# Optimization experiments

Hardware: AMD Instinct MI355X
Metric: run time of the kernel (lower is better)

The kernel has to match this reference:

```python
import jax, jax.numpy as jnp
import numpy as np
from jax import lax

B, N, G, K, D = 32, 32768, 64, 32, 384
EPS = 1e-5


def _fps(xyz, npoint):
    # Farthest point sampling; deterministic start at index 0 (original uses randint).
    b, n, _ = xyz.shape
    def step(carry, _):
        distance, farthest = carry
        centroid = jnp.take_along_axis(xyz, farthest[:, None, None], axis=1)  # (B,1,3)
        dist = jnp.sum((xyz - centroid) ** 2, axis=-1)                        # (B,N)
        distance = jnp.minimum(distance, dist)
        new_far = jnp.argmax(distance, axis=-1)
        return (distance, new_far), farthest
    init = (jnp.full((b, n), 1e10, xyz.dtype), jnp.zeros((b,), jnp.int32))
    _, cents = lax.scan(step, init, None, length=npoint)  # (npoint, B)
    return cents.T  # (B, npoint)


def _bn(h, g, bta, m, v):
    # inference-mode BatchNorm over channel (last) dim
    return (h - m) * (g * lax.rsqrt(v + EPS)) + bta


def setup_inputs() -> dict:
    key = jax.random.key(0)
    ks = jax.random.split(key, 5)
    xyz = jax.random.normal(ks[0], (B, N, 3), jnp.float32)
    features = jax.random.normal(ks[1], (B, N, 3), jnp.float32)
    w1 = jax.random.normal(ks[2], (64, 6), jnp.float32) * 0.1
    w2 = jax.random.normal(ks[3], (128, 64), jnp.float32) * 0.1
    w3 = jax.random.normal(ks[4], (D, 128), jnp.float32) * 0.1
    def bn(c):
        return jnp.ones((c,), jnp.float32), jnp.zeros((c,), jnp.float32), jnp.zeros((c,), jnp.float32), jnp.ones((c,), jnp.float32)
    g1, b1, m1, v1 = bn(64)
    g2, b2, m2, v2 = bn(128)
    g3, b3, m3, v3 = bn(D)
    return dict(xyz=xyz, features=features, w1=w1, g1=g1, b1=b1, m1=m1, v1=v1,
                w2=w2, g2=g2, b2=b2, m2=m2, v2=v2, w3=w3, g3=g3, b3=b3, m3=m3, v3=v3)


def reference(xyz, features, w1, g1, b1, m1, v1, w2, g2, b2, m2, v2, w3, g3, b3, m3, v3):
    fps_idx = _fps(xyz, G)                                           # (B,G)
    center = jnp.take_along_axis(xyz, fps_idx[:, :, None], axis=1)   # (B,G,3)
    # KNN via squared distances (same ordering as torch.cdist euclidean)
    xn2 = jnp.sum(xyz * xyz, axis=-1)                                # (B,N)
    cn2 = jnp.sum(center * center, axis=-1)                          # (B,G)
    d2 = cn2[:, :, None] + xn2[:, None, :] - 2.0 * jnp.einsum('bgc,bnc->bgn', center, xyz)
    _, knn_idx = lax.top_k(-d2, K)                                   # (B,G,K)
    gx = jax.vmap(lambda x, i: x[i])(xyz, knn_idx)                   # (B,G,K,3)
    gf = jax.vmap(lambda f, i: f[i])(features, knn_idx)              # (B,G,K,3)
    h = jnp.concatenate([gx - center[:, :, None, :], gf], axis=-1)   # (B,G,K,6)
    h = jax.nn.relu(_bn(jnp.einsum('bgkc,oc->bgko', h, w1), g1, b1, m1, v1))
    h = jax.nn.relu(_bn(jnp.einsum('bgkc,oc->bgko', h, w2), g2, b2, m2, v2))
    h = _bn(jnp.einsum('bgkc,oc->bgko', h, w3), g3, b3, m3, v3)      # (B,G,K,D)
    patch = jnp.max(h, axis=2)                                       # (B,G,D) adaptive max pool
    return center, patch
```

## Files before the change

### kernel.cpp

```cpp
#include <hip/hip_runtime.h>
#include <hip/hip_bf16.h>

#define BB 32
#define NN 32768
#define GG 64
#define KK 32
#define DD 384
#define EPSF 1e-5f
#define FPS_NBLK 8
#define FPS_SL   (NN/FPS_NBLK)

typedef __attribute__((ext_vector_type(8))) short short8;
typedef __attribute__((ext_vector_type(4))) float f32x4;

__device__ __forceinline__ float rn_add(float a, float b){ return __fadd_rn(a,b); }
__device__ __forceinline__ float rn_sub(float a, float b){ return __fsub_rn(a,b); }
__device__ __forceinline__ float rn_mul(float a, float b){ return __fmul_rn(a,b); }

__device__ __forceinline__ unsigned fkey(float d){
  unsigned u = __float_as_uint(d);
  return (u & 0x80000000u) ? ~u : (u | 0x80000000u);
}

__device__ __forceinline__ unsigned short f2bf(float f){
  unsigned u = __float_as_uint(f);
  unsigned r = (u + 0x7FFFu + ((u >> 16) & 1u)) >> 16;
  return (unsigned short)r;
}

#define REP16(X) X(0) X(1) X(2) X(3) X(4) X(5) X(6) X(7) \
                 X(8) X(9) X(10) X(11) X(12) X(13) X(14) X(15)

__device__ float g_center[BB*GG*3];
__device__ int   g_knn[BB*GG*KK];
__device__ float g_w1t[6*64];
__device__ float g_b1[64];
__device__ float g_b2[128];
__device__ float g_b3[384];
__device__ __align__(16) unsigned short g_w2f[8*2*64*8];
__device__ __align__(16) unsigned short g_w3f[24*4*64*8];
__device__ float g_X[BB*NN];
__device__ float g_Y[BB*NN];
__device__ float g_Z[BB*NN];
__device__ float g_N2[BB*NN];
__device__ unsigned long long g_part[BB*FPS_NBLK*GG];

__global__ __launch_bounds__(256) void k_soa(const float* __restrict__ xyz){
  int tid = blockIdx.x * blockDim.x + threadIdx.x;
  int b = tid >> 15;
  int p = tid & (NN - 1);
  const float* s = xyz + (size_t)b*NN*3 + (size_t)p*3;
  float x = s[0], y = s[1], z = s[2];
  g_X[tid] = x;
  g_Y[tid] = y;
  g_Z[tid] = z;
  g_N2[tid] = rn_add(rn_add(rn_mul(x,x), rn_mul(y,y)), rn_mul(z,z));
}

__global__ __launch_bounds__(256) void k_zero(void){
  int tid = blockIdx.x * blockDim.x + threadIdx.x;
  if (tid < BB*FPS_NBLK*GG) g_part[tid] = 0ull;
}

__global__ void k_prep(const float* __restrict__ w1, const float* __restrict__ g1, const float* __restrict__ b1, const float* __restrict__ m1, const float* __restrict__ v1,
                       const float* __restrict__ w2, const float* __restrict__ g2, const float* __restrict__ b2, const float* __restrict__ m2, const float* __restrict__ v2,
                       const float* __restrict__ w3, const float* __restrict__ g3, const float* __restrict__ b3, const float* __restrict__ m3, const float* __restrict__ v3){
  int tid = blockIdx.x * blockDim.x + threadIdx.x;
  int nt  = gridDim.x * blockDim.x;
  for (int e = tid; e < 64*6; e += nt){
    int c = e >> 6, o = e & 63;
    float s = g1[o] * rsqrtf(v1[o] + EPSF);
    g_w1t[e] = w1[o*6 + c] * s;
  }
  for (int o = tid; o < 64; o += nt){
    float s = g1[o] * rsqrtf(v1[o] + EPSF);
    g_b1[o] = b1[o] - m1[o]*s;
  }
  for (int o = tid; o < 128; o += nt){
    float s = g2[o] * rsqrtf(v2[o] + EPSF);
    g_b2[o] = b2[o] - m2[o]*s;
  }
  for (int o = tid; o < 384; o += nt){
    float s = g3[o] * rsqrtf(v3[o] + EPSF);
    g_b3[o] = b3[o] - m3[o]*s;
  }
  for (int idx = tid; idx < 8192; idx += nt){
    int e  = idx & 7;
    int l  = (idx >> 3) & 63;
    int kt = (idx >> 9) & 1;
    int ct = idx >> 10;
    int j  = ct*16 + (l & 15);
    int k  = kt*32 + ((l >> 4) << 3) + e;
    float s = g2[j] * rsqrtf(v2[j] + EPSF);
    g_w2f[idx] = f2bf(w2[j*64 + k] * s);
  }
  for (int idx = tid; idx < 49152; idx += nt){
    int e  = idx & 7;
    int l  = (idx >> 3) & 63;
    int kt = (idx >> 9) & 3;
    int ct = idx >> 11;
    int j  = ct*16 + (l & 15);
    int k  = kt*32 + ((l >> 4) << 3) + e;
    float s = g3[j] * rsqrtf(v3[j] + EPSF);
    g_w3f[idx] = f2bf(w3[j*128 + k] * s);
  }
}

__global__ __launch_bounds__(256)
void k_fps(float* __restrict__ outCenter){
  const int blk = blockIdx.x;
  const int b   = blk & 31;
  const int sub = blk >> 5;
  const int t   = threadIdx.x;
  const int wv  = t >> 6, ln = t & 63;
  const int base = sub * FPS_SL;
  const float* Xb = g_X + (size_t)b*NN;
  const float* Yb = g_Y + (size_t)b*NN;
  const float* Zb = g_Z + (size_t)b*NN;

  __shared__ float sx[FPS_SL], sy[FPS_SL], szz[FPS_SL];
  __shared__ unsigned long long skey[4];
  __shared__ int s_far;

  #pragma unroll
  for (int i = 0; i < 16; ++i){
    int p = (i << 8) + t;
    sx[p]  = Xb[base + p];
    sy[p]  = Yb[base + p];
    szz[p] = Zb[base + p];
  }
  __syncthreads();

#define DD_DECL(i) float dd##i = 1e10f;
  REP16(DD_DECL)
#undef DD_DECL

  int far = 0;
  for (int it = 0; ; ++it){
    if (sub == 0 && t == 0){
      float cx = Xb[far], cy = Yb[far], cz = Zb[far];
      float* cw = g_center  + (size_t)(b*GG + it)*3;
      float* co = outCenter + (size_t)(b*GG + it)*3;
      cw[0] = cx; cw[1] = cy; cw[2] = cz;
      co[0] = cx; co[1] = cy; co[2] = cz;
    }
    if (it == GG - 1) break;

    float cx = Xb[far], cy = Yb[far], cz = Zb[far];
    unsigned long long bk = 0ull;
#define DD_UPD(i) { \
    int p = (i << 8) + t; \
    float dx = rn_sub(sx[p], cx); \
    float dy = rn_sub(sy[p], cy); \
    float dz = rn_sub(szz[p], cz); \
    float s_ = rn_add(rn_add(rn_mul(dx,dx), rn_mul(dy,dy)), rn_mul(dz,dz)); \
    float d_ = fminf(dd##i, s_); \
    dd##i = d_; \
    unsigned long long k_ = ((unsigned long long)fkey(d_) << 32) \
                          | (unsigned)(0xFFFFFFFFu - (unsigned)(base + p)); \
    if (k_ > bk) bk = k_; }
    REP16(DD_UPD)
#undef DD_UPD

    #pragma unroll
    for (int off = 32; off >= 1; off >>= 1){
      unsigned long long o = (unsigned long long)__shfl_xor((long long)bk, off);
      if (o > bk) bk = o;
    }
    if (ln == 0) skey[wv] = bk;
    __syncthreads();
    if (wv == 0){
      unsigned long long m = (ln < 4) ? skey[ln] : 0ull;
      #pragma unroll
      for (int off = 1; off <= 2; off <<= 1){
        unsigned long long o = (unsigned long long)__shfl_xor((long long)m, off);
        if (o > m) m = o;
      }
      if (ln == 0)
        __hip_atomic_store(&g_part[(((b << 3) + sub) << 6) + it], m,
                           __ATOMIC_RELAXED, __HIP_MEMORY_SCOPE_AGENT);
      unsigned long long k = 0ull;
      if (ln < 8){
        unsigned long long* p = &g_part[(((b << 3) + ln) << 6) + it];
        do {
          k = __hip_atomic_load(p, __ATOMIC_RELAXED, __HIP_MEMORY_SCOPE_AGENT);
        } while (k == 0ull);
      }
      #pragma unroll
      for (int off = 1; off <= 4; off <<= 1){
        unsigned long long o = (unsigned long long)__shfl_xor((long long)k, off);
        if (o > k) k = o;
      }
      if (ln == 0) s_far = (int)(0xFFFFFFFFu - (unsigned)(k & 0xFFFFFFFFu));
    }
    __syncthreads();
    far = s_far;
  }
}

__global__ __launch_bounds__(256) void k_knn(void){
  const int bg = blockIdx.x;
  const int b  = bg >> 6;
  const int t  = threadIdx.x;
  const int w  = t >> 6;
  const int ln = t & 63;
  const float4* X4 = (const float4*)(g_X  + (size_t)b*NN);
  const float4* Y4 = (const float4*)(g_Y  + (size_t)b*NN);
  const float4* Z4 = (const float4*)(g_Z  + (size_t)b*NN);
  const float4* N4 = (const float4*)(g_N2 + (size_t)b*NN);

  __shared__ unsigned sE[64];
  __shared__ unsigned long long s_cand[512];
  __shared__ int s_cnt;

  const float* cp = g_center + (size_t)bg*3;
  float cx = cp[0], cy = cp[1], cz = cp[2];
  float cn2 = rn_add(rn_add(rn_mul(cx,cx), rn_mul(cy,cy)), rn_mul(cz,cz));

  float e0 = INFINITY, e1 = INFINITY;
  #pragma unroll 2
  for (int s = 0; s < 32; ++s){
    int q = (s << 8) + t;
    float4 x = X4[q], y = Y4[q], z = Z4[q], n = N4[q];
    #define D2C(c) { \
      float e = rn_add(rn_add(rn_mul(cx,x.c), rn_mul(cy,y.c)), rn_mul(cz,z.c)); \
      float d = rn_sub(rn_add(cn2, n.c), rn_add(e,e)); \
      if (d < e1){ if (d < e0){ e1 = e0; e0 = d; } else e1 = d; } }
    D2C(x) D2C(y) D2C(z) D2C(w)
    #undef D2C
  }

  {
    unsigned v = fkey(e1);
    #pragma unroll
    for (int k = 2; k <= 64; k <<= 1){
      #pragma unroll
      for (int j = k >> 1; j > 0; j >>= 1){
        unsigned o = (unsigned)__shfl_xor((int)v, j);
        bool keepmin = (((ln & k) == 0) == ((ln & j) == 0));
        unsigned mn = o < v ? o : v;
        unsigned mx = o < v ? v : o;
        v = keepmin ? mn : mx;
      }
    }
    if (ln < 16) sE[w*16 + ln] = v;
  }
  if (t == 0) s_cnt = 0;
  __syncthreads();

  unsigned T;
  {
    unsigned v = sE[ln];
    #pragma unroll
    for (int k = 2; k <= 64; k <<= 1){
      #pragma unroll
      for (int j = k >> 1; j > 0; j >>= 1){
        unsigned o = (unsigned)__shfl_xor((int)v, j);
        bool keepmin = (((ln & k) == 0) == ((ln & j) == 0));
        unsigned mn = o < v ? o : v;
        unsigned mx = o < v ? v : o;
        v = keepmin ? mn : mx;
      }
    }
    T = (unsigned)__shfl((int)v, 15);
  }

  #pragma unroll 2
  for (int s = 0; s < 32; ++s){
    int q = (s << 8) + t;
    float4 x = X4[q], y = Y4[q], z = Z4[q], n = N4[q];
    #define COLC(c, kk) { \
      float e = rn_add(rn_add(rn_mul(cx,x.c), rn_mul(cy,y.c)), rn_mul(cz,z.c)); \
      float d = rn_sub(rn_add(cn2, n.c), rn_add(e,e)); \
      unsigned fk = fkey(d); \
      if (fk <= T){ \
        int p = atomicAdd(&s_cnt, 1); \
        if (p < 512) \
          s_cand[p] = ((unsigned long long)fk << 32) | (unsigned)((q<<2)+kk); } }
    COLC(x,0) COLC(y,1) COLC(z,2) COLC(w,3)
    #undef COLC
  }
  __syncthreads();

  if (w == 0){
    int C = s_cnt; if (C > 512) C = 512;
    int* kout = g_knn + (size_t)bg*KK;
    if (C <= 64){
      unsigned long long kk = (ln < C) ? s_cand[ln] : ~0ull;
      #pragma unroll
      for (int k = 2; k <= 64; k <<= 1){
        #pragma unroll
        for (int j = k >> 1; j > 0; j >>= 1){
          unsigned long long o = (unsigned long long)__shfl_xor((long long)kk, j);
          bool keepmin = (((ln & k) == 0) == ((ln & j) == 0));
          unsigned long long mn = o < kk ? o : kk;
          unsigned long long mx = o < kk ? kk : o;
          kk = keepmin ? mn : mx;
        }
      }
      if (ln < KK) kout[ln] = (int)(kk & 0xffffffffu);
    } else {
      unsigned long long md[8];
      #pragma unroll
      for (int j = 0; j < 8; ++j){
        int e = ln + (j << 6);
        md[j] = (e < C) ? s_cand[e] : ~0ull;
      }
      for (int r = 0; r < KK; ++r){
        unsigned long long bk = md[0];
        #pragma unroll
        for (int j = 1; j < 8; ++j) if (md[j] < bk) bk = md[j];
        #pragma unroll
        for (int off = 32; off >= 1; off >>= 1){
          unsigned long long o = (unsigned long long)__shfl_xor((long long)bk, off);
          if (o < bk) bk = o;
        }
        #pragma unroll
        for (int j = 0; j < 8; ++j) if (md[j] == bk) md[j] = ~0ull;
        if (ln == 0) kout[r] = (int)(bk & 0xffffffffu);
      }
    }
  }
}

__global__ __launch_bounds__(256) void k_mlp(const float* __restrict__ xyz,
                                             const float* __restrict__ feat,
                                             float* __restrict__ outPatch){
  const int bg = blockIdx.x;
  const int b  = bg >> 6;
  const int t  = threadIdx.x;
  const int w  = t >> 6;
  const int ln = t & 63;
  const float* xb = xyz  + (size_t)b*NN*3;
  const float* fb = feat + (size_t)b*NN*3;

  __shared__ float h0[KK][8];
  __shared__ __align__(16) unsigned short h1b[KK][72];
  __shared__ __align__(16) unsigned short h2b[KK][136];

  if (t < KK){
    int idx = g_knn[(size_t)bg*KK + t] & (NN - 1);
    const float* cp = g_center + (size_t)bg*3;
    h0[t][0] = rn_sub(xb[idx*3+0], cp[0]);
    h0[t][1] = rn_sub(xb[idx*3+1], cp[1]);
    h0[t][2] = rn_sub(xb[idx*3+2], cp[2]);
    h0[t][3] = fb[idx*3+0];
    h0[t][4] = fb[idx*3+1];
    h0[t][5] = fb[idx*3+2];
  }
  __syncthreads();

  {
    int p = t >> 3, ob = (t & 7) * 8;
    float acc[8];
    #pragma unroll
    for (int j = 0; j < 8; ++j) acc[j] = g_b1[ob + j];
    #pragma unroll
    for (int c = 0; c < 6; ++c){
      float a = h0[p][c];
      const float4* wr = (const float4*)(g_w1t + c*64 + ob);
      float4 wa = wr[0], wb = wr[1];
      acc[0] = fmaf(a, wa.x, acc[0]); acc[1] = fmaf(a, wa.y, acc[1]);
      acc[2] = fmaf(a, wa.z, acc[2]); acc[3] = fmaf(a, wa.w, acc[3]);
      acc[4] = fmaf(a, wb.x, acc[4]); acc[5] = fmaf(a, wb.y, acc[5]);
      acc[6] = fmaf(a, wb.z, acc[6]); acc[7] = fmaf(a, wb.w, acc[7]);
    }
    short8 v;
    #pragma unroll
    for (int j = 0; j < 8; ++j) v[j] = (short)f2bf(fmaxf(acc[j], 0.f));
    *reinterpret_cast<short8*>(&h1b[p][ob]) = v;
  }
  __syncthreads();

  {
    f32x4 a00 = {0,0,0,0}, a01 = {0,0,0,0}, a10 = {0,0,0,0}, a11 = {0,0,0,0};
    const int g8 = (ln >> 4) << 3;
    #pragma unroll
    for (int kk = 0; kk < 2; ++kk){
      short8 A0 = *reinterpret_cast<const short8*>(&h1b[(ln & 15)][kk*32 + g8]);
      short8 A1 = *reinterpret_cast<const short8*>(&h1b[16 + (ln & 15)][kk*32 + g8]);
      short8 B0 = *reinterpret_cast<const short8*>(&g_w2f[(((2*w+0)*2 + kk)*64 + ln)*8]);
      short8 B1 = *reinterpret_cast<const short8*>(&g_w2f[(((2*w+1)*2 + kk)*64 + ln)*8]);
      a00 = __builtin_amdgcn_mfma_f32_16x16x32_bf16(A0, B0, a00, 0, 0, 0);
      a01 = __builtin_amdgcn_mfma_f32_16x16x32_bf16(A1, B0, a01, 0, 0, 0);
      a10 = __builtin_amdgcn_mfma_f32_16x16x32_bf16(A0, B1, a10, 0, 0, 0);
      a11 = __builtin_amdgcn_mfma_f32_16x16x32_bf16(A1, B1, a11, 0, 0, 0);
    }
    int col0 = (2*w)*16 + (ln & 15);
    int col1 = col0 + 16;
    float bz0 = g_b2[col0], bz1 = g_b2[col1];
    int r0 = (ln >> 4) << 2;
    #pragma unroll
    for (int r = 0; r < 4; ++r){
      h2b[r0 + r][col0]      = f2bf(fmaxf(a00[r] + bz0, 0.f));
      h2b[16 + r0 + r][col0] = f2bf(fmaxf(a01[r] + bz0, 0.f));
      h2b[r0 + r][col1]      = f2bf(fmaxf(a10[r] + bz1, 0.f));
      h2b[16 + r0 + r][col1] = f2bf(fmaxf(a11[r] + bz1, 0.f));
    }
  }
  __syncthreads();

  {
    f32x4 acc3[6][2];
    #pragma unroll
    for (int ci = 0; ci < 6; ++ci){
      acc3[ci][0] = (f32x4){0,0,0,0};
      acc3[ci][1] = (f32x4){0,0,0,0};
    }
    const int g8 = (ln >> 4) << 3;
    #pragma unroll
    for (int kk = 0; kk < 4; ++kk){
      short8 A0 = *reinterpret_cast<const short8*>(&h2b[(ln & 15)][kk*32 + g8]);
      short8 A1 = *reinterpret_cast<const short8*>(&h2b[16 + (ln & 15)][kk*32 + g8]);
      #pragma unroll
      for (int ci = 0; ci < 6; ++ci){
        int ct = w*6 + ci;
        short8 B = *reinterpret_cast<const short8*>(&g_w3f[((ct*4 + kk)*64 + ln)*8]);
        acc3[ci][0] = __builtin_amdgcn_mfma_f32_16x16x32_bf16(A0, B, acc3[ci][0], 0, 0, 0);
        acc3[ci][1] = __builtin_amdgcn_mfma_f32_16x16x32_bf16(A1, B, acc3[ci][1], 0, 0, 0);
      }
    }
    #pragma unroll
    for (int ci = 0; ci < 6; ++ci){
      float m = acc3[ci][0][0];
      #pragma unroll
      for (int r = 1; r < 4; ++r) m = fmaxf(m, acc3[ci][0][r]);
      #pragma unroll
      for (int r = 0; r < 4; ++r) m = fmaxf(m, acc3[ci][1][r]);
      m = fmaxf(m, __shfl_xor(m, 16));
      m = fmaxf(m, __shfl_xor(m, 32));
      if (ln < 16){
        int col = (w*6 + ci)*16 + ln;
        outPatch[(size_t)bg*DD + col] = m + g_b3[col];
      }
    }
  }
}

extern "C" void kernel_launch(void* const* d_in, const int* in_sizes, int n_in,
                              void* d_out, int out_size, void* d_ws, size_t ws_size,
                              hipStream_t stream){
  (void)in_sizes; (void)n_in; (void)out_size; (void)d_ws; (void)ws_size;
  const float* xyz  = (const float*)d_in[0];
  const float* feat = (const float*)d_in[1];
  const float* w1 = (const float*)d_in[2];
  const float* g1 = (const float*)d_in[3];
  const float* b1 = (const float*)d_in[4];
  const float* m1 = (const float*)d_in[5];
  const float* v1 = (const float*)d_in[6];
  const float* w2 = (const float*)d_in[7];
  const float* g2 = (const float*)d_in[8];
  const float* b2 = (const float*)d_in[9];
  const float* m2 = (const float*)d_in[10];
  const float* v2 = (const float*)d_in[11];
  const float* w3 = (const float*)d_in[12];
  const float* g3 = (const float*)d_in[13];
  const float* b3 = (const float*)d_in[14];
  const float* m3 = (const float*)d_in[15];
  const float* v3 = (const float*)d_in[16];
  float* out = (float*)d_out;

  k_prep<<<64, 256, 0, stream>>>(w1,g1,b1,m1,v1, w2,g2,b2,m2,v2, w3,g3,b3,m3,v3);
  k_soa<<<(BB*NN)/256, 256, 0, stream>>>(xyz);
  k_zero<<<64, 256, 0, stream>>>();
  k_fps<<<BB*FPS_NBLK, 256, 0, stream>>>(out);
  k_knn<<<BB*GG, 256, 0, stream>>>();
  k_mlp<<<BB*GG, 256, 0, stream>>>(xyz, feat, out + (size_t)BB*GG*3);
}
```

Measured before the change: 279.7 us.

## Pass centroid coordinates through tagged double-buffered FPS slots, use 512-thread blocks

The farthest-point-sampling kernel now publishes each block's winning point coordinates together with its key in a small double-buffered slot tagged by iteration. Other blocks then read the centroid directly from the slot instead of doing a dependent global load of X/Y/Z after the cross-block reduction. Blocks grow to 512 threads with 8 points per thread, which halves the serial per-thread loop. The iteration tag shrinks the index field to 15 bits, and correctness now depends on the release/acquire ordering and on slot reuse across alternating iterations.

```diff
diff --git a/kernel.cpp b/kernel.cpp
--- a/kernel.cpp
+++ b/kernel.cpp
@@ -28,8 +28,7 @@
   return (unsigned short)r;
 }
 
-#define REP16(X) X(0) X(1) X(2) X(3) X(4) X(5) X(6) X(7) \
-                 X(8) X(9) X(10) X(11) X(12) X(13) X(14) X(15)
+#define REP8(X) X(0) X(1) X(2) X(3) X(4) X(5) X(6) X(7)
 
 __device__ float g_center[BB*GG*3];
 __device__ int   g_knn[BB*GG*KK];
@@ -43,7 +42,7 @@
 __device__ float g_Y[BB*NN];
 __device__ float g_Z[BB*NN];
 __device__ float g_N2[BB*NN];
-__device__ unsigned long long g_part[BB*FPS_NBLK*GG];
+__device__ unsigned long long g_slot[BB*FPS_NBLK*2*16];
 
 __global__ __launch_bounds__(256) void k_soa(const float* __restrict__ xyz){
   int tid = blockIdx.x * blockDim.x + threadIdx.x;
@@ -59,7 +58,7 @@
 
 __global__ __launch_bounds__(256) void k_zero(void){
   int tid = blockIdx.x * blockDim.x + threadIdx.x;
-  if (tid < BB*FPS_NBLK*GG) g_part[tid] = 0ull;
+  if (tid < BB*FPS_NBLK*2*16) g_slot[tid] = 0ull;
 }
 
 __global__ void k_prep(const float* __restrict__ w1, const float* __restrict__ g1, const float* __restrict__ b1, const float* __restrict__ m1, const float* __restrict__ v1,
@@ -106,7 +105,7 @@
   }
 }
 
-__global__ __launch_bounds__(256)
+__global__ __launch_bounds__(512)
 void k_fps(float* __restrict__ outCenter){
   const int blk = blockIdx.x;
   const int b   = blk & 31;
@@ -119,12 +118,13 @@
   const float* Zb = g_Z + (size_t)b*NN;
 
   __shared__ float sx[FPS_SL], sy[FPS_SL], szz[FPS_SL];
-  __shared__ unsigned long long skey[4];
+  __shared__ unsigned long long skey[8];
   __shared__ int s_far;
+  __shared__ float s_cx, s_cy, s_cz;
 
   #pragma unroll
-  for (int i = 0; i < 16; ++i){
-    int p = (i << 8) + t;
+  for (int i = 0; i < 8; ++i){
+    int p = (i << 9) + t;
     sx[p]  = Xb[base + p];
     sy[p]  = Yb[base + p];
     szz[p] = Zb[base + p];
@@ -132,13 +132,14 @@
   __syncthreads();
 
 #define DD_DECL(i) float dd##i = 1e10f;
-  REP16(DD_DECL)
+  REP8(DD_DECL)
 #undef DD_DECL
 
-  int far = 0;
+  int   far = 0;
+  float cx = Xb[0], cy = Yb[0], cz = Zb[0];
+
   for (int it = 0; ; ++it){
     if (sub == 0 && t == 0){
-      float cx = Xb[far], cy = Yb[far], cz = Zb[far];
       float* cw = g_center  + (size_t)(b*GG + it)*3;
       float* co = outCenter + (size_t)(b*GG + it)*3;
       cw[0] = cx; cw[1] = cy; cw[2] = cz;
@@ -146,10 +147,10 @@
     }
     if (it == GG - 1) break;
 
-    float cx = Xb[far], cy = Yb[far], cz = Zb[far];
+    const unsigned long long tag = (unsigned long long)((unsigned)(it + 1) << 15);
     unsigned long long bk = 0ull;
 #define DD_UPD(i) { \
-    int p = (i << 8) + t; \
+    int p = (i << 9) + t; \
     float dx = rn_sub(sx[p], cx); \
     float dy = rn_sub(sy[p], cy); \
     float dz = rn_sub(szz[p], cz); \
@@ -157,9 +158,9 @@
     float d_ = fminf(dd##i, s_); \
     dd##i = d_; \
     unsigned long long k_ = ((unsigned long long)fkey(d_) << 32) \
-                          | (unsigned)(0xFFFFFFFFu - (unsigned)(base + p)); \
+                          | tag | (unsigned)(32767 - (base + p)); \
     if (k_ > bk) bk = k_; }
-    REP16(DD_UPD)
+    REP8(DD_UPD)
 #undef DD_UPD
 
     #pragma unroll
@@ -170,31 +171,48 @@
     if (ln == 0) skey[wv] = bk;
     __syncthreads();
     if (wv == 0){
-      unsigned long long m = (ln < 4) ? skey[ln] : 0ull;
-      #pragma unroll
-      for (int off = 1; off <= 2; off <<= 1){
+      unsigned long long m = (ln < 8) ? skey[ln] : 0ull;
+      #pragma unroll
+      for (int off = 1; off <= 4; off <<= 1){
         unsigned long long o = (unsigned long long)__shfl_xor((long long)m, off);
         if (o > m) m = o;
       }
-      if (ln == 0)
-        __hip_atomic_store(&g_part[(((b << 3) + sub) << 6) + it], m,
-                           __ATOMIC_RELAXED, __HIP_MEMORY_SCOPE_AGENT);
-      unsigned long long k = 0ull;
+      if (ln == 0){
+        int pl = (32767 - (int)(m & 0x7FFFu)) - base;
+        unsigned long long xy = ((unsigned long long)__float_as_uint(sx[pl]) << 32)
+                              | (unsigned long long)__float_as_uint(sy[pl]);
+        unsigned long long zz = (unsigned long long)__float_as_uint(szz[pl]);
+        unsigned long long* S = &g_slot[((((b << 3) + sub) << 1) + (it & 1)) << 4];
+        __hip_atomic_store(S + 1, xy, __ATOMIC_RELAXED, __HIP_MEMORY_SCOPE_AGENT);
+        __hip_atomic_store(S + 2, zz, __ATOMIC_RELAXED, __HIP_MEMORY_SCOPE_AGENT);
+        __hip_atomic_store(S + 0, m,  __ATOMIC_RELEASE, __HIP_MEMORY_SCOPE_AGENT);
+      }
+      unsigned long long k = 0ull, xy = 0ull, zz = 0ull;
       if (ln < 8){
-        unsigned long long* p = &g_part[(((b << 3) + ln) << 6) + it];
+        unsigned long long* S = &g_slot[((((b << 3) + ln) << 1) + (it & 1)) << 4];
         do {
-          k = __hip_atomic_load(p, __ATOMIC_RELAXED, __HIP_MEMORY_SCOPE_AGENT);
-        } while (k == 0ull);
+          k = __hip_atomic_load(S + 0, __ATOMIC_ACQUIRE, __HIP_MEMORY_SCOPE_AGENT);
+        } while ((((unsigned)k) >> 15) != (unsigned)(it + 1));
+        xy = __hip_atomic_load(S + 1, __ATOMIC_RELAXED, __HIP_MEMORY_SCOPE_AGENT);
+        zz = __hip_atomic_load(S + 2, __ATOMIC_RELAXED, __HIP_MEMORY_SCOPE_AGENT);
       }
       #pragma unroll
       for (int off = 1; off <= 4; off <<= 1){
-        unsigned long long o = (unsigned long long)__shfl_xor((long long)k, off);
-        if (o > k) k = o;
-      }
-      if (ln == 0) s_far = (int)(0xFFFFFFFFu - (unsigned)(k & 0xFFFFFFFFu));
+        unsigned long long ok  = (unsigned long long)__shfl_xor((long long)k,  off);
+        unsigned long long oxy = (unsigned long long)__shfl_xor((long long)xy, off);
+        unsigned long long ozz = (unsigned long long)__shfl_xor((long long)zz, off);
+        if (ok > k){ k = ok; xy = oxy; zz = ozz; }
+      }
+      if (ln == 0){
+        s_far = 32767 - (int)(k & 0x7FFFu);
+        s_cx = __uint_as_float((unsigned)(xy >> 32));
+        s_cy = __uint_as_float((unsigned)(xy & 0xFFFFFFFFu));
+        s_cz = __uint_as_float((unsigned)(zz & 0xFFFFFFFFu));
+      }
     }
     __syncthreads();
-    far = s_far;
+    far = s_far; cx = s_cx; cy = s_cy; cz = s_cz;
+    (void)far;
   }
 }
 
@@ -463,7 +481,7 @@
   k_prep<<<64, 256, 0, stream>>>(w1,g1,b1,m1,v1, w2,g2,b2,m2,v2, w3,g3,b3,m3,v3);
   k_soa<<<(BB*NN)/256, 256, 0, stream>>>(xyz);
   k_zero<<<64, 256, 0, stream>>>();
-  k_fps<<<BB*FPS_NBLK, 256, 0, stream>>>(out);
+  k_fps<<<BB*FPS_NBLK, 512, 0, stream>>>(out);
   k_knn<<<BB*GG, 256, 0, stream>>>();
   k_mlp<<<BB*GG, 256, 0, stream>>>(xyz, feat, out + (size_t)BB*GG*3);
 }
```

Result: slower. 536.5 us (+91.8%).
